# Performance work log

Hardware: AMD Instinct MI355X
Metric: run time of the kernel (lower is better)

The kernel has to match this reference:

```python
import jax, jax.numpy as jnp
import numpy as np

N, L, D, H = 2, 2048, 1024, 16
Dh = D // H          # 64
HIST = 2048          # history_len
SCALE = D ** 0.5     # note: module scales by sqrt(model_dim), not sqrt(head_dim)


def setup_inputs() -> dict:
    key = jax.random.key(0)
    ks = jax.random.split(key, 10)
    f = lambda k, s, sc=1.0: jax.random.normal(k, s, dtype=jnp.float32) * sc
    i = jnp.arange(L)
    causal = i[None, :] > i[:, None]            # mask future
    old = i[None, :] <= i[:, None] - HIST       # mask beyond history window
    mask = causal | old                          # True = masked, (L, L)
    return {
        "values": f(ks[0], (N, L, D)),
        "keys": f(ks[1], (N, L, D)),
        "query": f(ks[2], (N, L, D)),
        "origin_values": f(ks[3], (N, L, D)),
        "origin_keys": f(ks[4], (N, L, D)),
        "Wv": f(ks[5], (Dh, Dh), 0.1),
        "Wk": f(ks[6], (Dh, Dh), 0.1),
        "Wq": f(ks[7], (Dh, Dh), 0.1),
        "fc_w": f(ks[8], (D, D), 0.03),
        "fc_b": jnp.zeros((D,), dtype=jnp.float32),
        "mask": mask,
    }


def reference(values, keys, query, origin_values, origin_keys, Wv, Wk, Wq, fc_w, fc_b, mask):
    # forward(..., ref_sample=True): mfpca_attention path.
    # origin_keys/values are projected exactly as the prior ref_sample=False call stored them.
    split = lambda x: x.reshape(N, L, H, Dh)
    v = split(values) @ Wv.T        # (N, L, H, Dh)  torch Linear: x @ W^T, no bias
    k = split(keys) @ Wk.T
    q = split(query) @ Wq.T
    ov = split(origin_values) @ Wv.T
    ok = split(origin_keys) @ Wk.T

    energy = jnp.einsum('nqhd,nkhd->nhqk', q, ok)       # (N, H, L, L)
    samp_energy = jnp.einsum('nlhd,nlhd->nhl', q, k)    # (N, H, L)
    eye = jnp.eye(L, dtype=bool)
    # energy.diagonal().copy_(samp_energy)
    energy = jnp.where(eye, samp_energy[:, :, None, :], energy)
    energy = jnp.where(mask, jnp.float32(-1e20), energy)
    scores = jax.nn.softmax(energy / SCALE, axis=-1)
    diag_scores = jnp.diagonal(scores, axis1=2, axis2=3)    # (N, H, L)
    scores_nodiag = jnp.where(eye, 0.0, scores)
    # NOTE: original einsum output is indexed by l (not q) -- reproduced faithfully.
    origin_attention = jnp.einsum('nhql,nlhd->nlhd', scores_nodiag, ov)
    samp_attention = jnp.einsum('nhl,nlhd->nlhd', diag_scores, v)
    attention = (samp_attention + origin_attention).reshape(N, L, D)
    return attention @ fc_w.T + fc_b
```

## Files before the change

kernel.cpp:

```cpp
#include <hip/hip_runtime.h>

#define NB 2
#define LL 2048
#define DD 1024
#define HH 16
#define NHH (NB*HH)
#define LT (LL/64)
#define KT16 (LL/16)
#define CEXP 0.0450842200277801f

typedef __bf16 bf16x8 __attribute__((ext_vector_type(8)));
typedef unsigned short u16x8 __attribute__((ext_vector_type(8)));
typedef float f32x4 __attribute__((ext_vector_type(4)));

#define MFMA16 __builtin_amdgcn_mfma_f32_16x16x32_bf16
#define EXP2 __builtin_amdgcn_exp2f

__device__ __forceinline__ unsigned short f2bf(float f) {
    unsigned u = __float_as_uint(f);
    return (unsigned short)((u + 0x7fffu + ((u >> 16) & 1u)) >> 16);
}
__device__ __forceinline__ float bf2f(unsigned short u) {
    return __uint_as_float(((unsigned)u) << 16);
}
__device__ __forceinline__ bf16x8 ldfrag(const unsigned short* p) {
    return *reinterpret_cast<const bf16x8*>(p);
}
__device__ __forceinline__ bf16x8 cvt8v(float4 a, float4 b) {
    u16x8 u;
    u[0]=f2bf(a.x); u[1]=f2bf(a.y); u[2]=f2bf(a.z); u[3]=f2bf(a.w);
    u[4]=f2bf(b.x); u[5]=f2bf(b.y); u[6]=f2bf(b.z); u[7]=f2bf(b.w);
    return __builtin_bit_cast(bf16x8, u);
}
__device__ __forceinline__ ushort4 pack4(f32x4 d, float sc) {
    ushort4 o;
    o.x = f2bf(d[0]*sc); o.y = f2bf(d[1]*sc); o.z = f2bf(d[2]*sc); o.w = f2bf(d[3]*sc);
    return o;
}
__device__ __forceinline__ void gload16(const unsigned short* g, unsigned short* l) {
    __builtin_amdgcn_global_load_lds(
        (const __attribute__((address_space(1))) unsigned int*)g,
        (__attribute__((address_space(3))) unsigned int*)l, 16, 0, 0);
}

__global__ __launch_bounds__(256) void prep_kernel(
    const float* __restrict__ Wk, const float* __restrict__ Wq,
    const float* __restrict__ Wv, unsigned short* __restrict__ wfrag,
    const float* __restrict__ fc_w, unsigned short* __restrict__ fcwb,
    float* __restrict__ zreg)
{
    const int bid = blockIdx.x;
    const int t = threadIdx.x;
    if (bid < 6) {
        const int s = bid * 256 + t;
        const int m = s >> 9;
        const int rem = s & 511;
        const int f = rem >> 6;
        const int lane = rem & 63;
        const int n16 = lane & 15, quad = lane >> 4;
        const int mt = f >> 1, half = f & 1;
        const float* W = (m == 0) ? Wk : (m == 1) ? Wq : Wv;
        const float* p = W + (mt*16 + n16)*64 + quad*8 + half*32;
        float4 a = *reinterpret_cast<const float4*>(p);
        float4 b = *reinterpret_cast<const float4*>(p + 4);
        *reinterpret_cast<bf16x8*>(wfrag + (size_t)s * 8) = cvt8v(a, b);
    } else if (bid < 6 + 1024) {
        const int idx = (bid - 6) * 1024 + t * 4;
        float4 wv = *reinterpret_cast<const float4*>(fc_w + idx);
        ushort4 o;
        o.x = f2bf(wv.x); o.y = f2bf(wv.y); o.z = f2bf(wv.z); o.w = f2bf(wv.w);
        *reinterpret_cast<ushort4*>(fcwb + idx) = o;
    } else {
        const int i = (bid - 1030) * 1024 + t * 4;
        *reinterpret_cast<float4*>(zreg + i) = (float4){0.f, 0.f, 0.f, 0.f};
    }
}

__global__ __launch_bounds__(256) void proj_kernel(
    const float* __restrict__ values, const float* __restrict__ keys,
    const float* __restrict__ query,  const float* __restrict__ ovals,
    const float* __restrict__ okeys,  const unsigned short* __restrict__ wfrag,
    unsigned short* __restrict__ qb, unsigned short* __restrict__ okb,
    unsigned short* __restrict__ vb, unsigned short* __restrict__ ovb,
    float* __restrict__ ediag)
{
    const int t = threadIdx.x;
    const int w = t >> 6;
    const int lane = t & 63;
    const int n16 = lane & 15;
    const int quad = lane >> 4;
    const int h = blockIdx.y;
    const int row = blockIdx.x * 64 + w * 16 + n16;
    const int nn = row >> 11;
    const int ll = row & 2047;
    const size_t xoff  = (size_t)row * DD + h * 64 + quad * 8;
    const size_t qbase = (((size_t)(nn * HH + h)) * LL + ll) * 64;
    const size_t vbase = (size_t)row * DD + h * 64;

    if (blockIdx.z == 0) {
        const float4* kp = reinterpret_cast<const float4*>(keys  + xoff);
        const float4* qp = reinterpret_cast<const float4*>(query + xoff);
        const float4* op = reinterpret_cast<const float4*>(okeys + xoff);
        float4 k0 = kp[0], k1 = kp[1], k2 = kp[8], k3 = kp[9];
        float4 q0 = qp[0], q1 = qp[1], q2 = qp[8], q3 = qp[9];
        float4 o0 = op[0], o1 = op[1], o2 = op[8], o3 = op[9];
        bf16x8 wk[8], wq[8];
#pragma unroll
        for (int f = 0; f < 8; ++f) {
            wk[f] = ldfrag(wfrag + (size_t)(f * 64 + lane) * 8);
            wq[f] = ldfrag(wfrag + (size_t)((8 + f) * 64 + lane) * 8);
        }
        bf16x8 xk0 = cvt8v(k0, k1), xk1 = cvt8v(k2, k3);
        bf16x8 xq0 = cvt8v(q0, q1), xq1 = cvt8v(q2, q3);
        bf16x8 xo0 = cvt8v(o0, o1), xo1 = cvt8v(o2, o3);
        f32x4 ka[4], qa[4];
#pragma unroll
        for (int mt = 0; mt < 4; ++mt) {
            f32x4 d = {0.f,0.f,0.f,0.f};
            d = MFMA16(wk[mt*2], xk0, d, 0,0,0);
            ka[mt] = MFMA16(wk[mt*2+1], xk1, d, 0,0,0);
        }
#pragma unroll
        for (int mt = 0; mt < 4; ++mt) {
            f32x4 d = {0.f,0.f,0.f,0.f};
            d = MFMA16(wq[mt*2], xq0, d, 0,0,0);
            qa[mt] = MFMA16(wq[mt*2+1], xq1, d, 0,0,0);
            *reinterpret_cast<ushort4*>(qb + qbase + mt*16 + quad*4) = pack4(qa[mt], CEXP);
        }
#pragma unroll
        for (int mt = 0; mt < 4; ++mt) {
            f32x4 d = {0.f,0.f,0.f,0.f};
            d = MFMA16(wk[mt*2], xo0, d, 0,0,0);
            d = MFMA16(wk[mt*2+1], xo1, d, 0,0,0);
            *reinterpret_cast<ushort4*>(okb + qbase + mt*16 + quad*4) = pack4(d, 1.0f);
        }
        float p = 0.f;
#pragma unroll
        for (int mt = 0; mt < 4; ++mt)
            p += qa[mt][0]*ka[mt][0] + qa[mt][1]*ka[mt][1]
               + qa[mt][2]*ka[mt][2] + qa[mt][3]*ka[mt][3];
        p += __shfl_xor(p, 16);
        p += __shfl_xor(p, 32);
        if (lane < 16)
            ediag[((size_t)(nn * HH + h)) * LL + ll] = p;
    } else {
        const float4* vp = reinterpret_cast<const float4*>(values + xoff);
        const float4* op = reinterpret_cast<const float4*>(ovals  + xoff);
        float4 v0 = vp[0], v1 = vp[1], v2 = vp[8], v3 = vp[9];
        float4 o0 = op[0], o1 = op[1], o2 = op[8], o3 = op[9];
        bf16x8 wv[8];
#pragma unroll
        for (int f = 0; f < 8; ++f)
            wv[f] = ldfrag(wfrag + (size_t)((16 + f) * 64 + lane) * 8);
        bf16x8 xv0 = cvt8v(v0, v1), xv1 = cvt8v(v2, v3);
        bf16x8 xo0 = cvt8v(o0, o1), xo1 = cvt8v(o2, o3);
#pragma unroll
        for (int mt = 0; mt < 4; ++mt) {
            f32x4 d = {0.f,0.f,0.f,0.f};
            d = MFMA16(wv[mt*2], xv0, d, 0,0,0);
            d = MFMA16(wv[mt*2+1], xv1, d, 0,0,0);
            *reinterpret_cast<ushort4*>(vb + vbase + mt*16 + quad*4) = pack4(d, 1.0f);
        }
#pragma unroll
        for (int mt = 0; mt < 4; ++mt) {
            f32x4 d = {0.f,0.f,0.f,0.f};
            d = MFMA16(wv[mt*2], xo0, d, 0,0,0);
            d = MFMA16(wv[mt*2+1], xo1, d, 0,0,0);
            *reinterpret_cast<ushort4*>(ovb + vbase + mt*16 + quad*4) = pack4(d, 1.0f);
        }
    }
}

__global__ __launch_bounds__(256) void zrow_part(
    const unsigned short* __restrict__ qb, const unsigned short* __restrict__ okb,
    float* __restrict__ Zbuf)
{
    const int px = blockIdx.x;
    const int pair = px >> 1;
    const int s = px & 1;
    const int nh = blockIdx.y;
    const int t = threadIdx.x;
    const int w = t >> 6;
    const int lane = t & 63;
    const int n = lane & 15;
    const int quad = lane >> 4;
    const size_t base = (size_t)nh * (LL * 64);
    const size_t nhL = (size_t)nh * LL;
    const int r0 = 4 * s + w;

#pragma unroll
    for (int half = 0; half < 2; ++half) {
        const int qt = half ? (31 - pair) : pair;
        const int kend = 4 * qt + 4;

        bf16x8 bq[4][2];
#pragma unroll
        for (int ct = 0; ct < 4; ++ct) {
            const unsigned short* p = qb + base + (size_t)(qt*64 + ct*16 + n) * 64 + quad * 8;
            bq[ct][0] = ldfrag(p); bq[ct][1] = ldfrag(p + 32);
        }

        float zacc[4] = {0.f, 0.f, 0.f, 0.f};

        bf16x8 a0A = {}, a1A = {}, a0B = {}, a1B = {}, a0C = {}, a1C = {};
        if (r0 < kend) {
            const unsigned short* p = okb + base + (size_t)(r0*16 + n) * 64 + quad * 8;
            a0A = ldfrag(p); a1A = ldfrag(p + 32);
        }
        if (r0 + 8 < kend) {
            const unsigned short* p = okb + base + (size_t)((r0+8)*16 + n) * 64 + quad * 8;
            a0B = ldfrag(p); a1B = ldfrag(p + 32);
        }
        if (r0 + 16 < kend) {
            const unsigned short* p = okb + base + (size_t)((r0+16)*16 + n) * 64 + quad * 8;
            a0C = ldfrag(p); a1C = ldfrag(p + 32);
        }
        for (int kt = r0; kt < kend; kt += 8) {
            bf16x8 a0 = a0A, a1 = a1A;
            a0A = a0B; a1A = a1B; a0B = a0C; a1B = a1C;
            if (kt + 24 < kend) {
                const unsigned short* p = okb + base + (size_t)((kt+24)*16 + n) * 64 + quad * 8;
                a0C = ldfrag(p); a1C = ldfrag(p + 32);
            }
            const int dk = kt - 4*qt;
#pragma unroll
            for (int ct = 0; ct < 4; ++ct) {
                if (ct < dk) continue;
                f32x4 d = {0.f,0.f,0.f,0.f};
                d = MFMA16(a0, bq[ct][0], d, 0,0,0);
                d = MFMA16(a1, bq[ct][1], d, 0,0,0);
                if (ct == dk) {
#pragma unroll
                    for (int r = 0; r < 4; ++r)
                        if (quad*4 + r < n) zacc[ct] += EXP2(d[r]);
                } else {
#pragma unroll
                    for (int r = 0; r < 4; ++r) zacc[ct] += EXP2(d[r]);
                }
            }
        }

#pragma unroll
        for (int ct = 0; ct < 4; ++ct) {
            float z = zacc[ct];
            z += __shfl_down(z, 32);
            z += __shfl_down(z, 16);
            if (lane < 16)
                atomicAdd(&Zbuf[nhL + qt*64 + ct*16 + lane], z);
        }
    }
}

__global__ __launch_bounds__(256) void zfin_kernel(
    const float* __restrict__ Zbuf, const float* __restrict__ ediag,
    float* __restrict__ invZ, float* __restrict__ diag_s)
{
    const int i = blockIdx.x * 256 + threadIdx.x;
    const float de = EXP2(ediag[i] * CEXP);
    const float iz = 1.f / (Zbuf[i] + de);
    invZ[i]   = iz;
    diag_s[i] = de * iz;
}

__global__ __launch_bounds__(256) void colsum_part(
    const unsigned short* __restrict__ qb, const unsigned short* __restrict__ okb,
    const float* __restrict__ invZ, float* __restrict__ colsum)
{
    const int px = blockIdx.x;
    const int pair = px >> 1;
    const int s = px & 1;
    const int nh = blockIdx.y;
    const int t = threadIdx.x;
    const int w = t >> 6;
    const int lane = t & 63;
    const int n = lane & 15;
    const int quad = lane >> 4;
    const size_t base = (size_t)nh * (LL * 64);
    const size_t nhL = (size_t)nh * LL;
    const int r0 = 4 * s + w;

#pragma unroll
    for (int half = 0; half < 2; ++half) {
        const int lt = half ? (31 - pair) : pair;

        bf16x8 bl[4][2];
#pragma unroll
        for (int ct = 0; ct < 4; ++ct) {
            const unsigned short* p = okb + base + (size_t)(lt*64 + ct*16 + n) * 64 + quad * 8;
            bl[ct][0] = ldfrag(p); bl[ct][1] = ldfrag(p + 32);
        }

        float cacc[4] = {0.f, 0.f, 0.f, 0.f};

        const int kstart = 4*lt + r0;
        bf16x8 a0A = {}, a1A = {}, a0B = {}, a1B = {}, a0C = {}, a1C = {};
        float4 izA = {0,0,0,0}, izB = {0,0,0,0}, izC = {0,0,0,0};
        if (kstart < KT16) {
            const unsigned short* p = qb + base + (size_t)(kstart*16 + n) * 64 + quad * 8;
            a0A = ldfrag(p); a1A = ldfrag(p + 32);
            izA = *reinterpret_cast<const float4*>(invZ + nhL + kstart*16 + quad*4);
        }
        if (kstart + 8 < KT16) {
            const unsigned short* p = qb + base + (size_t)((kstart+8)*16 + n) * 64 + quad * 8;
            a0B = ldfrag(p); a1B = ldfrag(p + 32);
            izB = *reinterpret_cast<const float4*>(invZ + nhL + (kstart+8)*16 + quad*4);
        }
        if (kstart + 16 < KT16) {
            const unsigned short* p = qb + base + (size_t)((kstart+16)*16 + n) * 64 + quad * 8;
            a0C = ldfrag(p); a1C = ldfrag(p + 32);
            izC = *reinterpret_cast<const float4*>(invZ + nhL + (kstart+16)*16 + quad*4);
        }
        for (int kt = kstart; kt < KT16; kt += 8) {
            bf16x8 a0 = a0A, a1 = a1A; const float4 izv = izA;
            a0A = a0B; a1A = a1B; izA = izB;
            a0B = a0C; a1B = a1C; izB = izC;
            if (kt + 24 < KT16) {
                const unsigned short* p = qb + base + (size_t)((kt+24)*16 + n) * 64 + quad * 8;
                a0C = ldfrag(p); a1C = ldfrag(p + 32);
                izC = *reinterpret_cast<const float4*>(invZ + nhL + (kt+24)*16 + quad*4);
            }
            const int dk = kt - 4*lt;
#pragma unroll
            for (int ct = 0; ct < 4; ++ct) {
                if (ct > dk) continue;
                f32x4 d = {0.f,0.f,0.f,0.f};
                d = MFMA16(a0, bl[ct][0], d, 0,0,0);
                d = MFMA16(a1, bl[ct][1], d, 0,0,0);
                if (ct == dk) {
                    if (quad*4 + 0 > n) cacc[ct] += EXP2(d[0]) * izv.x;
                    if (quad*4 + 1 > n) cacc[ct] += EXP2(d[1]) * izv.y;
                    if (quad*4 + 2 > n) cacc[ct] += EXP2(d[2]) * izv.z;
                    if (quad*4 + 3 > n) cacc[ct] += EXP2(d[3]) * izv.w;
                } else {
                    cacc[ct] += EXP2(d[0]) * izv.x;
                    cacc[ct] += EXP2(d[1]) * izv.y;
                    cacc[ct] += EXP2(d[2]) * izv.z;
                    cacc[ct] += EXP2(d[3]) * izv.w;
                }
            }
        }

#pragma unroll
        for (int ct = 0; ct < 4; ++ct) {
            float c = cacc[ct];
            c += __shfl_down(c, 32);
            c += __shfl_down(c, 16);
            if (lane < 16)
                atomicAdd(&colsum[nhL + lt*64 + ct*16 + lane], c);
        }
    }
}

#define LOADA(vS, ovS, dsS, csS, k) do {                                   \
    vS  = ldfrag(pv  + (k)*32);                                            \
    ovS = ldfrag(pov + (k)*32);                                            \
    dsS = diag_s[scbase + ((k)>>1)*LL];                                    \
    csS = colsum[scbase + ((k)>>1)*LL];                                    \
} while (0)

#define CVTWRITE(vS, ovS, dsS, csS, dst) do {                              \
    u16x8 vu_ = __builtin_bit_cast(u16x8, vS);                             \
    u16x8 ou_ = __builtin_bit_cast(u16x8, ovS);                            \
    u16x8 o_;                                                              \
    _Pragma("unroll")                                                      \
    for (int i_ = 0; i_ < 8; ++i_)                                         \
        o_[i_] = f2bf(dsS * bf2f(vu_[i_]) + csS * bf2f(ou_[i_]));          \
    *reinterpret_cast<u16x8*>(dst) = o_;                                   \
} while (0)

#define COMPUTE(Abuf, Bbuf) do {                                           \
    bf16x8 af_[4], bf_[2];                                                 \
    _Pragma("unroll")                                                      \
    for (int mt = 0; mt < 4; ++mt)                                         \
        af_[mt] = ldfrag((Abuf) + (wr*64 + mt*16 + n)*32 + quad*8);        \
    _Pragma("unroll")                                                      \
    for (int nt = 0; nt < 2; ++nt)                                         \
        bf_[nt] = ldfrag((Bbuf) + (wc*32 + nt*16 + n)*32 + quad*8);        \
    _Pragma("unroll")                                                      \
    for (int mt = 0; mt < 4; ++mt)                                         \
        _Pragma("unroll")                                                  \
        for (int nt = 0; nt < 2; ++nt)                                     \
            acc[mt][nt] = MFMA16(af_[mt], bf_[nt], acc[mt][nt], 0,0,0);    \
} while (0)

__global__ __launch_bounds__(512) void out_kernel(
    const unsigned short* __restrict__ vb, const unsigned short* __restrict__ ovb,
    const float* __restrict__ diag_s, const float* __restrict__ colsum,
    const unsigned short* __restrict__ fcwb, const float* __restrict__ fc_b,
    float* __restrict__ out)
{
    __shared__ unsigned short lds[2][2][128 * 32];

    const int bid = blockIdx.x;
    const int swz = (bid & 7) * 32 + (bid >> 3);
    const int ct = swz & 7;
    const int rt = swz >> 3;
    const int row0 = rt * 128, col0 = ct * 128;

    const int t = threadIdx.x;
    const int w = t >> 6, lane = t & 63;
    const int n = lane & 15, quad = lane >> 4;
    const int wr = w >> 2, wc = w & 3;

    const int arow = row0 + (t >> 2);
    const unsigned short* pv  = vb  + (size_t)arow * DD + (t & 3) * 8;
    const unsigned short* pov = ovb + (size_t)arow * DD + (t & 3) * 8;
    const int scbase = (arow >> 11) * (HH * LL) + (arow & 2047);
    const unsigned short* gb = fcwb + (size_t)(col0 + (t >> 2)) * DD + (t & 3) * 8;
    unsigned short* la0 = &lds[0][0][t * 8];
    unsigned short* lb0 = &lds[0][1][t * 8];
    unsigned short* la1 = &lds[1][0][t * 8];
    unsigned short* lb1 = &lds[1][1][t * 8];
    const unsigned short* A0 = &lds[0][0][0];
    const unsigned short* B0 = &lds[0][1][0];
    const unsigned short* A1 = &lds[1][0][0];
    const unsigned short* B1 = &lds[1][1][0];

    f32x4 acc[4][2];
#pragma unroll
    for (int mt = 0; mt < 4; ++mt)
#pragma unroll
        for (int nt = 0; nt < 2; ++nt) acc[mt][nt] = (f32x4){0.f, 0.f, 0.f, 0.f};

    bf16x8 vP, ovP, vQ, ovQ; float dsP, csP, dsQ, csQ;
    LOADA(vP, ovP, dsP, csP, 0);
    LOADA(vQ, ovQ, dsQ, csQ, 1);
    gload16(gb, lb0);
    CVTWRITE(vP, ovP, dsP, csP, la0);
    __syncthreads();

    for (int kt = 0; kt < 32; kt += 2) {
        gload16(gb + (kt + 1) * 32, lb1);
        if (kt + 2 < 32) LOADA(vP, ovP, dsP, csP, kt + 2);
        COMPUTE(A0, B0);
        CVTWRITE(vQ, ovQ, dsQ, csQ, la1);
        __syncthreads();
        if (kt + 2 < 32) {
            gload16(gb + (kt + 2) * 32, lb0);
            if (kt + 3 < 32) LOADA(vQ, ovQ, dsQ, csQ, kt + 3);
        }
        COMPUTE(A1, B1);
        if (kt + 2 < 32) CVTWRITE(vP, ovP, dsP, csP, la0);
        __syncthreads();
    }

#pragma unroll
    for (int nt = 0; nt < 2; ++nt) {
        const int col = col0 + wc * 32 + nt * 16 + n;
        const float bias = fc_b[col];
#pragma unroll
        for (int mt = 0; mt < 4; ++mt)
#pragma unroll
            for (int r = 0; r < 4; ++r)
                out[(size_t)(row0 + wr * 64 + mt * 16 + quad * 4 + r) * DD + col]
                    = acc[mt][nt][r] + bias;
    }
}

extern "C" void kernel_launch(void* const* d_in, const int* in_sizes, int n_in,
                              void* d_out, int out_size, void* d_ws, size_t ws_size,
                              hipStream_t stream) {
    const float* values = (const float*)d_in[0];
    const float* keys   = (const float*)d_in[1];
    const float* query  = (const float*)d_in[2];
    const float* ovals  = (const float*)d_in[3];
    const float* okeys  = (const float*)d_in[4];
    const float* Wv     = (const float*)d_in[5];
    const float* Wk     = (const float*)d_in[6];
    const float* Wq     = (const float*)d_in[7];
    const float* fc_w   = (const float*)d_in[8];
    const float* fc_b   = (const float*)d_in[9];
    float* out = (float*)d_out;

    float* ws      = (float*)d_ws;
    float* ediag   = ws;
    float* Zbuf    = ediag + 65536;
    float* colsum  = Zbuf + 65536;
    float* invZ    = colsum + 65536;
    float* diag_s  = invZ + 65536;
    unsigned short* qb   = (unsigned short*)(diag_s + 65536);
    unsigned short* okb  = qb   + 4194304;
    unsigned short* vb   = okb  + 4194304;
    unsigned short* ovb  = vb   + 4194304;
    unsigned short* fcwb = ovb  + 4194304;
    unsigned short* wfrag = fcwb + 1048576;

    prep_kernel<<<dim3(1158), 256, 0, stream>>>(Wk, Wq, Wv, wfrag, fc_w, fcwb, Zbuf);
    proj_kernel<<<dim3(64, 16, 2), 256, 0, stream>>>(
        values, keys, query, ovals, okeys, wfrag, qb, okb, vb, ovb, ediag);
    zrow_part<<<dim3(32, NHH), 256, 0, stream>>>(qb, okb, Zbuf);
    zfin_kernel<<<dim3(256), 256, 0, stream>>>(Zbuf, ediag, invZ, diag_s);
    colsum_part<<<dim3(32, NHH), 256, 0, stream>>>(qb, okb, invZ, colsum);
    out_kernel<<<dim3(256), 512, 0, stream>>>(vb, ovb, diag_s, colsum, fcwb, fc_b, out);
}
```

Measured before the change: 237.8 us.

## Fuse softmax normalizer into consumers and remap blocks for XCD locality

Removes the zfin kernel and recomputes 1/Z and the diagonal score inline, inside colsum_part and out_kernel, from Zbuf and ediag. This saves one launch and the invZ/diag_s write-read round trip, at the cost of redundant exp2 and reciprocal work in the inner loops. The zrow and colsum grids are also flattened to 1D and remapped so that all blocks of a given head land on the same XCD (bid&7). This is meant to improve L2 reuse of that head's q/ok data.

```diff
diff --git a/kernel.cpp b/kernel.cpp
--- a/kernel.cpp
+++ b/kernel.cpp
@@ -175,10 +175,13 @@
     const unsigned short* __restrict__ qb, const unsigned short* __restrict__ okb,
     float* __restrict__ Zbuf)
 {
-    const int px = blockIdx.x;
+    const int bid = blockIdx.x;
+    const int xcd = bid & 7;
+    const int slot = bid >> 3;
+    const int nh = xcd * 4 + (slot >> 5);
+    const int px = slot & 31;
     const int pair = px >> 1;
     const int s = px & 1;
-    const int nh = blockIdx.y;
     const int t = threadIdx.x;
     const int w = t >> 6;
     const int lane = t & 63;
@@ -251,25 +254,18 @@
     }
 }
 
-__global__ __launch_bounds__(256) void zfin_kernel(
-    const float* __restrict__ Zbuf, const float* __restrict__ ediag,
-    float* __restrict__ invZ, float* __restrict__ diag_s)
-{
-    const int i = blockIdx.x * 256 + threadIdx.x;
-    const float de = EXP2(ediag[i] * CEXP);
-    const float iz = 1.f / (Zbuf[i] + de);
-    invZ[i]   = iz;
-    diag_s[i] = de * iz;
-}
-
 __global__ __launch_bounds__(256) void colsum_part(
     const unsigned short* __restrict__ qb, const unsigned short* __restrict__ okb,
-    const float* __restrict__ invZ, float* __restrict__ colsum)
+    const float* __restrict__ Zbuf, const float* __restrict__ ediag,
+    float* __restrict__ colsum)
 {
-    const int px = blockIdx.x;
+    const int bid = blockIdx.x;
+    const int xcd = bid & 7;
+    const int slot = bid >> 3;
+    const int nh = xcd * 4 + (slot >> 5);
+    const int px = slot & 31;
     const int pair = px >> 1;
     const int s = px & 1;
-    const int nh = blockIdx.y;
     const int t = threadIdx.x;
     const int w = t >> 6;
     const int lane = t & 63;
@@ -294,31 +290,41 @@
 
         const int kstart = 4*lt + r0;
         bf16x8 a0A = {}, a1A = {}, a0B = {}, a1B = {}, a0C = {}, a1C = {};
-        float4 izA = {0,0,0,0}, izB = {0,0,0,0}, izC = {0,0,0,0};
+        float4 zA = {0,0,0,0}, zB = {0,0,0,0}, zC = {0,0,0,0};
+        float4 eA = {0,0,0,0}, eB = {0,0,0,0}, eC = {0,0,0,0};
         if (kstart < KT16) {
             const unsigned short* p = qb + base + (size_t)(kstart*16 + n) * 64 + quad * 8;
             a0A = ldfrag(p); a1A = ldfrag(p + 32);
-            izA = *reinterpret_cast<const float4*>(invZ + nhL + kstart*16 + quad*4);
+            zA = *reinterpret_cast<const float4*>(Zbuf  + nhL + kstart*16 + quad*4);
+            eA = *reinterpret_cast<const float4*>(ediag + nhL + kstart*16 + quad*4);
         }
         if (kstart + 8 < KT16) {
             const unsigned short* p = qb + base + (size_t)((kstart+8)*16 + n) * 64 + quad * 8;
             a0B = ldfrag(p); a1B = ldfrag(p + 32);
-            izB = *reinterpret_cast<const float4*>(invZ + nhL + (kstart+8)*16 + quad*4);
+            zB = *reinterpret_cast<const float4*>(Zbuf  + nhL + (kstart+8)*16 + quad*4);
+            eB = *reinterpret_cast<const float4*>(ediag + nhL + (kstart+8)*16 + quad*4);
         }
         if (kstart + 16 < KT16) {
             const unsigned short* p = qb + base + (size_t)((kstart+16)*16 + n) * 64 + quad * 8;
             a0C = ldfrag(p); a1C = ldfrag(p + 32);
-            izC = *reinterpret_cast<const float4*>(invZ + nhL + (kstart+16)*16 + quad*4);
+            zC = *reinterpret_cast<const float4*>(Zbuf  + nhL + (kstart+16)*16 + quad*4);
+            eC = *reinterpret_cast<const float4*>(ediag + nhL + (kstart+16)*16 + quad*4);
         }
         for (int kt = kstart; kt < KT16; kt += 8) {
-            bf16x8 a0 = a0A, a1 = a1A; const float4 izv = izA;
-            a0A = a0B; a1A = a1B; izA = izB;
-            a0B = a0C; a1B = a1C; izB = izC;
+            bf16x8 a0 = a0A, a1 = a1A; const float4 zv = zA, ev = eA;
+            a0A = a0B; a1A = a1B; zA = zB; eA = eB;
+            a0B = a0C; a1B = a1C; zB = zC; eB = eC;
             if (kt + 24 < KT16) {
                 const unsigned short* p = qb + base + (size_t)((kt+24)*16 + n) * 64 + quad * 8;
                 a0C = ldfrag(p); a1C = ldfrag(p + 32);
-                izC = *reinterpret_cast<const float4*>(invZ + nhL + (kt+24)*16 + quad*4);
+                zC = *reinterpret_cast<const float4*>(Zbuf  + nhL + (kt+24)*16 + quad*4);
+                eC = *reinterpret_cast<const float4*>(ediag + nhL + (kt+24)*16 + quad*4);
             }
+            float4 izv;
+            izv.x = 1.f / (zv.x + EXP2(ev.x * CEXP));
+            izv.y = 1.f / (zv.y + EXP2(ev.y * CEXP));
+            izv.z = 1.f / (zv.z + EXP2(ev.z * CEXP));
+            izv.w = 1.f / (zv.w + EXP2(ev.w * CEXP));
             const int dk = kt - 4*lt;
 #pragma unroll
             for (int ct = 0; ct < 4; ++ct) {
@@ -351,20 +357,23 @@
     }
 }
 
-#define LOADA(vS, ovS, dsS, csS, k) do {                                   \
+#define LOADA(vS, ovS, zS, eS, csS, k) do {                                \
     vS  = ldfrag(pv  + (k)*32);                                            \
     ovS = ldfrag(pov + (k)*32);                                            \
-    dsS = diag_s[scbase + ((k)>>1)*LL];                                    \
+    zS  = Zbuf  [scbase + ((k)>>1)*LL];                                    \
+    eS  = ediag [scbase + ((k)>>1)*LL];                                    \
     csS = colsum[scbase + ((k)>>1)*LL];                                    \
 } while (0)
 
-#define CVTWRITE(vS, ovS, dsS, csS, dst) do {                              \
+#define CVTWRITE(vS, ovS, zS, eS, csS, dst) do {                           \
+    const float de_ = EXP2(eS * CEXP);                                     \
+    const float ds_ = de_ * (1.f / (zS + de_));                            \
     u16x8 vu_ = __builtin_bit_cast(u16x8, vS);                             \
     u16x8 ou_ = __builtin_bit_cast(u16x8, ovS);                            \
     u16x8 o_;                                                              \
     _Pragma("unroll")                                                      \
     for (int i_ = 0; i_ < 8; ++i_)                                         \
-        o_[i_] = f2bf(dsS * bf2f(vu_[i_]) + csS * bf2f(ou_[i_]));          \
+        o_[i_] = f2bf(ds_ * bf2f(vu_[i_]) + csS * bf2f(ou_[i_]));          \
     *reinterpret_cast<u16x8*>(dst) = o_;                                   \
 } while (0)
 
@@ -385,7 +394,8 @@
 
 __global__ __launch_bounds__(512) void out_kernel(
     const unsigned short* __restrict__ vb, const unsigned short* __restrict__ ovb,
-    const float* __restrict__ diag_s, const float* __restrict__ colsum,
+    const float* __restrict__ Zbuf, const float* __restrict__ ediag,
+    const float* __restrict__ colsum,
     const unsigned short* __restrict__ fcwb, const float* __restrict__ fc_b,
     float* __restrict__ out)
 {
@@ -422,25 +432,25 @@
 #pragma unroll
         for (int nt = 0; nt < 2; ++nt) acc[mt][nt] = (f32x4){0.f, 0.f, 0.f, 0.f};
 
-    bf16x8 vP, ovP, vQ, ovQ; float dsP, csP, dsQ, csQ;
-    LOADA(vP, ovP, dsP, csP, 0);
-    LOADA(vQ, ovQ, dsQ, csQ, 1);
+    bf16x8 vP, ovP, vQ, ovQ; float zP, eP, csP, zQ, eQ, csQ;
+    LOADA(vP, ovP, zP, eP, csP, 0);
+    LOADA(vQ, ovQ, zQ, eQ, csQ, 1);
     gload16(gb, lb0);
-    CVTWRITE(vP, ovP, dsP, csP, la0);
+    CVTWRITE(vP, ovP, zP, eP, csP, la0);
     __syncthreads();
 
     for (int kt = 0; kt < 32; kt += 2) {
         gload16(gb + (kt + 1) * 32, lb1);
-        if (kt + 2 < 32) LOADA(vP, ovP, dsP, csP, kt + 2);
+        if (kt + 2 < 32) LOADA(vP, ovP, zP, eP, csP, kt + 2);
         COMPUTE(A0, B0);
-        CVTWRITE(vQ, ovQ, dsQ, csQ, la1);
+        CVTWRITE(vQ, ovQ, zQ, eQ, csQ, la1);
         __syncthreads();
         if (kt + 2 < 32) {
             gload16(gb + (kt + 2) * 32, lb0);
-            if (kt + 3 < 32) LOADA(vQ, ovQ, dsQ, csQ, kt + 3);
+            if (kt + 3 < 32) LOADA(vQ, ovQ, zQ, eQ, csQ, kt + 3);
         }
         COMPUTE(A1, B1);
-        if (kt + 2 < 32) CVTWRITE(vP, ovP, dsP, csP, la0);
+        if (kt + 2 < 32) CVTWRITE(vP, ovP, zP, eP, csP, la0);
         __syncthreads();
     }
 
@@ -476,9 +486,7 @@
     float* ediag   = ws;
     float* Zbuf    = ediag + 65536;
     float* colsum  = Zbuf + 65536;
-    float* invZ    = colsum + 65536;
-    float* diag_s  = invZ + 65536;
-    unsigned short* qb   = (unsigned short*)(diag_s + 65536);
+    unsigned short* qb   = (unsigned short*)(colsum + 65536);
     unsigned short* okb  = qb   + 4194304;
     unsigned short* vb   = okb  + 4194304;
     unsigned short* ovb  = vb   + 4194304;
@@ -488,8 +496,7 @@
     prep_kernel<<<dim3(1158), 256, 0, stream>>>(Wk, Wq, Wv, wfrag, fc_w, fcwb, Zbuf);
     proj_kernel<<<dim3(64, 16, 2), 256, 0, stream>>>(
         values, keys, query, ovals, okeys, wfrag, qb, okb, vb, ovb, ediag);
-    zrow_part<<<dim3(32, NHH), 256, 0, stream>>>(qb, okb, Zbuf);
-    zfin_kernel<<<dim3(256), 256, 0, stream>>>(Zbuf, ediag, invZ, diag_s);
-    colsum_part<<<dim3(32, NHH), 256, 0, stream>>>(qb, okb, invZ, colsum);
-    out_kernel<<<dim3(256), 512, 0, stream>>>(vb, ovb, diag_s, colsum, fcwb, fc_b, out);
-}
+    zrow_part<<<dim3(1024), 256, 0, stream>>>(qb, okb, Zbuf);
+    colsum_part<<<dim3(1024), 256, 0, stream>>>(qb, okb, Zbuf, ediag, colsum);
+    out_kernel<<<dim3(256), 512, 0, stream>>>(vb, ovb, Zbuf, ediag, colsum, fcwb, fc_b, out);
+}
```

Measured after the change: 247.3 us. +4.0%, slower.
